# Kernel tuning notes

Hardware: AMD Instinct MI355X
Metric: run time of the kernel (lower is better)

The kernel has to match this reference:

```python
import jax, jax.numpy as jnp
import numpy as np

ALPHA = 5.0
LAMBDA = 1.0


def setup_inputs() -> dict:
    key = jax.random.key(0)
    k1, k2 = jax.random.split(key)
    N, BITS, NCLASS = 2048, 64, 32
    b = jax.random.normal(k1, (N, BITS), dtype=jnp.float32)
    y = jax.random.randint(k2, (N,), 0, NCLASS, dtype=jnp.int32)
    return {"b": b, "y": y}


def reference(b, y):
    # similarity = 0.5 * <b_i, b_j>  -> [N, N]
    sim = 0.5 * (b @ b.T)
    # affinity: same-label pairs (equivalent to onehot(y) @ onehot(y).T > 0)
    aff = y[:, None] == y[None, :]  # [N, N] bool
    N = sim.shape[0]

    def step(carry, i):
        loss_sum, cnt = carry
        pos = aff[i]            # [N] bool, positives for row i
        theta = sim[i]          # [N]
        # triple[p, n] = theta_pos[p] - theta_neg[n] - alpha, clamped
        t = jnp.clip(theta[:, None] - theta[None, :] - ALPHA, -100.0, 50.0)
        # -(t - log(1 + exp(t))) == log1p(exp(t)) - t  (== softplus(-t))
        val = jnp.log1p(jnp.exp(t)) - t
        mask = pos[:, None] & (~pos)[None, :]
        npairs = mask.sum()
        valid = pos.any() & (~pos).any()
        row_loss = jnp.where(
            valid,
            jnp.where(mask, val, 0.0).sum() / jnp.maximum(npairs, 1).astype(val.dtype),
            0.0,
        )
        return (loss_sum + row_loss, cnt + valid.astype(jnp.float32)), None

    init = (jnp.float32(0.0), jnp.float32(0.0))
    (loss_sum, cnt), _ = jax.lax.scan(step, init, jnp.arange(N))
    loss1 = jnp.where(cnt > 0, loss_sum / jnp.maximum(cnt, 1.0), 0.0)
    # quantization loss (sign has zero gradient, same as torch)
    loss2 = jnp.mean((b - jnp.sign(b)) ** 2)
    total = loss1 + LAMBDA * loss2
    return total, loss1, loss2
```

## Files before the change

kernel.cpp:

```cpp
#include <hip/hip_runtime.h>
#include <math.h>

#define NROW 2048
#define BITS 64
#define MB 512
#define RPB 4
#define JQ 4
#define NBLK (NROW / RPB)
#define NWV (MB / 64)
#define MAXPOS 256

#define LN2_F   0.6931471805599453f
#define THSCALE 0.7213475204444817f
#define A_SC    7.213475204444817f

__global__ __launch_bounds__(256) void bt_kernel(const float* __restrict__ b,
                                                 float* __restrict__ bT)
{
    __shared__ float tile[64][65];
    const int t  = threadIdx.x;
    const int j0 = blockIdx.x * 64;
    {
        const int jj = t >> 2, q = t & 3;
        const float4* b4 = reinterpret_cast<const float4*>(b + (size_t)(j0 + jj) * BITS);
#pragma unroll
        for (int m = 0; m < 4; ++m) {
            const float4 v = b4[q * 4 + m];
            const int col = q * 16 + m * 4;
            tile[jj][col + 0] = v.x; tile[jj][col + 1] = v.y;
            tile[jj][col + 2] = v.z; tile[jj][col + 3] = v.w;
        }
    }
    __syncthreads();
    {
        const int k = t >> 2, q = t & 3;
#pragma unroll
        for (int s = 0; s < 4; ++s) {
            float4 v;
            v.x = tile[q * 16 + s * 4 + 0][k];
            v.y = tile[q * 16 + s * 4 + 1][k];
            v.z = tile[q * 16 + s * 4 + 2][k];
            v.w = tile[q * 16 + s * 4 + 3][k];
            *reinterpret_cast<float4*>(&bT[(size_t)k * NROW + j0 + q * 16 + s * 4]) = v;
        }
    }
}

__device__ __forceinline__ float slow4(float e, const float* __restrict__ pp)
{
    float s = 0.f;
#pragma unroll
    for (int k = 0; k < 4; ++k)
        s += __builtin_amdgcn_logf(fmaf(e, pp[k], 1.f));
    return s;
}

template <bool TR>
__global__ __launch_bounds__(MB) void dhn_main(
    const float* __restrict__ b, const float* __restrict__ bT,
    const int* __restrict__ y,
    float* __restrict__ blockLoss, float* __restrict__ blockValid,
    float* __restrict__ blockQ)
{
    const int br  = blockIdx.x;
    const int i0  = br * RPB;
    const int tid = threadIdx.x;
    const int w = tid >> 6, lane = tid & 63;

    __shared__ __align__(16) float  biT[BITS * RPB];
    __shared__ __align__(16) float  posPe[RPB][MAXPOS + 8];
    __shared__ __align__(16) float4 posSG[RPB][MAXPOS / 4 + 2];
    __shared__ int   waveTot[RPB][NWV];
    __shared__ int   waveBase[RPB][NWV];
    __shared__ int   pcnt[RPB];
    __shared__ float wred[NWV], wq[NWV];

    if (tid < BITS * RPB) {
        const int k = tid >> 2, r = tid & 3;
        biT[tid] = b[(size_t)(i0 + r) * BITS + k];
    }
    __syncthreads();

    float th[JQ][RPB] = {};
    if constexpr (TR) {
        const float4* bt4 = reinterpret_cast<const float4*>(bT);
        const float4* bi4 = reinterpret_cast<const float4*>(biT);
#pragma unroll 8
        for (int k = 0; k < BITS; ++k) {
            const float4 bj = bt4[k * (NROW / 4) + tid];
            const float4 bi = bi4[k];
            th[0][0] += bj.x * bi.x; th[0][1] += bj.x * bi.y;
            th[0][2] += bj.x * bi.z; th[0][3] += bj.x * bi.w;
            th[1][0] += bj.y * bi.x; th[1][1] += bj.y * bi.y;
            th[1][2] += bj.y * bi.z; th[1][3] += bj.y * bi.w;
            th[2][0] += bj.z * bi.x; th[2][1] += bj.z * bi.y;
            th[2][2] += bj.z * bi.z; th[2][3] += bj.z * bi.w;
            th[3][0] += bj.w * bi.x; th[3][1] += bj.w * bi.y;
            th[3][2] += bj.w * bi.z; th[3][3] += bj.w * bi.w;
        }
    } else {
        for (int k = 0; k < BITS; ++k) {
#pragma unroll
            for (int q = 0; q < JQ; ++q) {
                const float v = b[(size_t)(4 * tid + q) * BITS + k];
#pragma unroll
                for (int r = 0; r < RPB; ++r) th[q][r] += v * biT[k * 4 + r];
            }
        }
    }

    const int4 y4 = reinterpret_cast<const int4*>(y)[tid];
    const int yj[JQ] = { y4.x, y4.y, y4.z, y4.w };
    int yr[RPB];
#pragma unroll
    for (int r = 0; r < RPB; ++r) yr[r] = y[i0 + r];

    float ev[JQ][RPB];
    int pm[RPB], cnt[RPB];
#pragma unroll
    for (int r = 0; r < RPB; ++r) {
        int m = 0;
#pragma unroll
        for (int q = 0; q < JQ; ++q) {
            const float t2 = th[q][r] * THSCALE;
            const bool f = (yj[q] == yr[r]);
            ev[q][r] = __builtin_amdgcn_exp2f(f ? -t2 : t2 + A_SC);
            if (f) m |= 1 << q;
        }
        pm[r] = m;
        cnt[r] = __popc(m);
    }

    int excl[RPB];
#pragma unroll
    for (int r = 0; r < RPB; ++r) {
        int v = cnt[r];
#pragma unroll
        for (int off = 1; off < 64; off <<= 1) {
            const int t2 = __shfl_up(v, off);
            if (lane >= off) v += t2;
        }
        excl[r] = v - cnt[r];
        if (lane == 63) waveTot[r][w] = v;
    }
    __syncthreads();
    if (tid < RPB) {
        int base = 0;
#pragma unroll
        for (int wv = 0; wv < NWV; ++wv) { waveBase[tid][wv] = base; base += waveTot[tid][wv]; }
        pcnt[tid] = base;
    }
    __syncthreads();

#pragma unroll
    for (int r = 0; r < RPB; ++r) {
        int o = waveBase[r][w] + excl[r];
#pragma unroll
        for (int q = 0; q < JQ; ++q) {
            if ((pm[r] >> q) & 1) {
                if (o < MAXPOS) posPe[r][o] = ev[q][r];
                ++o;
            }
        }
    }
    if (tid < RPB * 8) {
        const int r = tid >> 3, q = tid & 7;
        const int P = pcnt[r] < MAXPOS ? pcnt[r] : MAXPOS;
        const int idx = P + q;
        if (idx < ((P + 7) & ~7)) posPe[r][idx] = 0.f;
    }
    __syncthreads();

    if (tid < RPB * (MAXPOS / 4)) {
        const int r = tid / (MAXPOS / 4);
        const int g = tid % (MAXPOS / 4);
        const int P = pcnt[r] < MAXPOS ? pcnt[r] : MAXPOS;
        const int Ppad = (P + 7) & ~7;
        if (g * 4 < Ppad) {
            float c1 = 0.f, c2 = 0.f, c3 = 0.f, c4 = 0.f;
#pragma unroll
            for (int k = 0; k < 4; ++k) {
                const float p = posPe[r][g * 4 + k];
                c4 = fmaf(p, c3, c4);
                c3 = fmaf(p, c2, c3);
                c2 = fmaf(p, c1, c2);
                c1 += p;
            }
            posSG[r][g] = make_float4(c1, c2, c3, c4);
        }
    }
    __syncthreads();

    float total = 0.f;
#pragma unroll
    for (int r = 0; r < RPB; ++r) {
        const int Pc = pcnt[r];
        const int P  = Pc < MAXPOS ? Pc : MAXPOS;
        const int PG = ((P + 7) & ~7) >> 3;
        float e[JQ];
#pragma unroll
        for (int q = 0; q < JQ; ++q)
            e[q] = ((pm[r] >> q) & 1) ? 0.f : ev[q][r];
        float a[JQ] = {};
        const float4* sg4 = &posSG[r][0];
        const float*  pp  = &posPe[r][0];
        for (int g = 0; g < PG; ++g) {
            const float4 A = sg4[2 * g + 0];
            const float4 B = sg4[2 * g + 1];
#pragma unroll
            for (int q = 0; q < JQ; ++q) {
                const float eq = e[q];
                const float hA = fmaf(fmaf(fmaf(fmaf(A.w, eq, A.z), eq, A.y), eq, A.x), eq, 1.f);
                float lA = __builtin_amdgcn_logf(hA);
                if (__builtin_expect(isinf(hA), 0)) lA = slow4(eq, pp + 8 * g);
                const float hB = fmaf(fmaf(fmaf(fmaf(B.w, eq, B.z), eq, B.y), eq, B.x), eq, 1.f);
                float lB = __builtin_amdgcn_logf(hB);
                if (__builtin_expect(isinf(hB), 0)) lB = slow4(eq, pp + 8 * g + 4);
                a[q] += lA + lB;
            }
        }
        const bool valid = (Pc > 0) && (Pc < NROW);
        const float denom = (float)Pc * (float)(NROW - Pc);
        total += valid ? ((a[0] + a[1]) + (a[2] + a[3])) / denom : 0.f;
    }
    total *= LN2_F;

    float q2 = 0.f;
    if (tid < BITS * RPB) {
        const float x  = biT[tid];
        const float sg = (x > 0.f) ? 1.f : ((x < 0.f) ? -1.f : 0.f);
        const float d  = x - sg;
        q2 = d * d;
    }

#pragma unroll
    for (int off = 32; off > 0; off >>= 1) {
        total += __shfl_xor(total, off);
        q2    += __shfl_xor(q2, off);
    }
    if (lane == 0) { wred[w] = total; wq[w] = q2; }
    __syncthreads();
    if (tid == 0) {
        float tl = 0.f, tq = 0.f;
#pragma unroll
        for (int v = 0; v < NWV; ++v) { tl += wred[v]; tq += wq[v]; }
        blockLoss[br] = tl;
        blockQ[br]    = tq;
        float vc = 0.f;
#pragma unroll
        for (int r = 0; r < RPB; ++r)
            vc += ((pcnt[r] > 0) && (pcnt[r] < NROW)) ? 1.f : 0.f;
        blockValid[br] = vc;
    }
}

__global__ __launch_bounds__(256) void dhn_final_kernel(
    const float* __restrict__ blockLoss, const float* __restrict__ blockValid,
    const float* __restrict__ blockQ, float* __restrict__ out)
{
    const int tid = threadIdx.x;
    const int w = tid >> 6, lane = tid & 63;
    __shared__ float r1[4], r2[4], r3[4];

    float sl = 0.f, sv = 0.f, sq = 0.f;
    for (int i = tid; i < NBLK; i += 256) {
        sl += blockLoss[i]; sv += blockValid[i]; sq += blockQ[i];
    }
#pragma unroll
    for (int off = 32; off > 0; off >>= 1) {
        sl += __shfl_xor(sl, off);
        sv += __shfl_xor(sv, off);
        sq += __shfl_xor(sq, off);
    }
    if (lane == 0) { r1[w] = sl; r2[w] = sv; r3[w] = sq; }
    __syncthreads();
    if (tid == 0) {
        float SL = 0.f, SV = 0.f, SQ = 0.f;
#pragma unroll
        for (int v = 0; v < 4; ++v) { SL += r1[v]; SV += r2[v]; SQ += r3[v]; }
        const float loss1 = (SV > 0.f) ? SL / fmaxf(SV, 1.f) : 0.f;
        const float loss2 = SQ / (float)(NROW * BITS);
        out[0] = loss1 + 1.0f * loss2;
        out[1] = loss1;
        out[2] = loss2;
    }
}

extern "C" void kernel_launch(void* const* d_in, const int* in_sizes, int n_in,
                              void* d_out, int out_size, void* d_ws, size_t ws_size,
                              hipStream_t stream) {
    const float* b = (const float*)d_in[0];
    const int*   y = (const int*)d_in[1];
    float* out = (float*)d_out;

    float* blockLoss  = (float*)d_ws;
    float* blockValid = (float*)((char*)d_ws + 4096);
    float* blockQ     = (float*)((char*)d_ws + 8192);
    float* bT         = (float*)((char*)d_ws + 16384);

    const size_t need = 16384 + (size_t)BITS * NROW * sizeof(float);
    if (ws_size >= need) {
        bt_kernel<<<NROW / 64, 256, 0, stream>>>(b, bT);
        dhn_main<true><<<NBLK, MB, 0, stream>>>(b, bT, y, blockLoss, blockValid, blockQ);
    } else {
        dhn_main<false><<<NBLK, MB, 0, stream>>>(b, nullptr, y, blockLoss, blockValid, blockQ);
    }
    dhn_final_kernel<<<1, 256, 0, stream>>>(blockLoss, blockValid, blockQ, out);
}
```

Before: 42.56 us.

## Batch four log2 evaluations into one via mantissa product and exponent sum

Widens the positive-group size from 8 to 16 and replaces four separate log2 calls per group with one. Each polynomial result is split into an integer exponent and a mantissa in [1,2). The four mantissas are multiplied and a single log2 is taken, while the exponents are summed as integers and corrected at the end. This cuts transcendental instruction count roughly fourfold in the hot loop, at the cost of extra integer/bit operations, more padding work, and a noinline slow fallback covering 16 elements when any value overflows to infinity.

```diff
diff --git a/kernel.cpp b/kernel.cpp
--- a/kernel.cpp
+++ b/kernel.cpp
@@ -46,11 +46,11 @@
     }
 }
 
-__device__ __forceinline__ float slow4(float e, const float* __restrict__ pp)
+__device__ __noinline__ float slow16(float e, const float* __restrict__ pp)
 {
     float s = 0.f;
 #pragma unroll
-    for (int k = 0; k < 4; ++k)
+    for (int k = 0; k < 16; ++k)
         s += __builtin_amdgcn_logf(fmaf(e, pp[k], 1.f));
     return s;
 }
@@ -68,8 +68,8 @@
     const int w = tid >> 6, lane = tid & 63;
 
     __shared__ __align__(16) float  biT[BITS * RPB];
-    __shared__ __align__(16) float  posPe[RPB][MAXPOS + 8];
-    __shared__ __align__(16) float4 posSG[RPB][MAXPOS / 4 + 2];
+    __shared__ __align__(16) float  posPe[RPB][MAXPOS + 16];
+    __shared__ __align__(16) float4 posSG[RPB][MAXPOS / 4 + 4];
     __shared__ int   waveTot[RPB][NWV];
     __shared__ int   waveBase[RPB][NWV];
     __shared__ int   pcnt[RPB];
@@ -163,11 +163,11 @@
             }
         }
     }
-    if (tid < RPB * 8) {
-        const int r = tid >> 3, q = tid & 7;
+    if (tid < RPB * 16) {
+        const int r = tid >> 4, q = tid & 15;
         const int P = pcnt[r] < MAXPOS ? pcnt[r] : MAXPOS;
         const int idx = P + q;
-        if (idx < ((P + 7) & ~7)) posPe[r][idx] = 0.f;
+        if (idx < ((P + 15) & ~15)) posPe[r][idx] = 0.f;
     }
     __syncthreads();
 
@@ -175,7 +175,7 @@
         const int r = tid / (MAXPOS / 4);
         const int g = tid % (MAXPOS / 4);
         const int P = pcnt[r] < MAXPOS ? pcnt[r] : MAXPOS;
-        const int Ppad = (P + 7) & ~7;
+        const int Ppad = (P + 15) & ~15;
         if (g * 4 < Ppad) {
             float c1 = 0.f, c2 = 0.f, c3 = 0.f, c4 = 0.f;
 #pragma unroll
@@ -196,32 +196,52 @@
     for (int r = 0; r < RPB; ++r) {
         const int Pc = pcnt[r];
         const int P  = Pc < MAXPOS ? Pc : MAXPOS;
-        const int PG = ((P + 7) & ~7) >> 3;
+        const int PG = ((P + 15) & ~15) >> 4;
         float e[JQ];
 #pragma unroll
         for (int q = 0; q < JQ; ++q)
             e[q] = ((pm[r] >> q) & 1) ? 0.f : ev[q][r];
         float a[JQ] = {};
+        int   ei[JQ] = {};
         const float4* sg4 = &posSG[r][0];
         const float*  pp  = &posPe[r][0];
         for (int g = 0; g < PG; ++g) {
-            const float4 A = sg4[2 * g + 0];
-            const float4 B = sg4[2 * g + 1];
+            const float4 A = sg4[4 * g + 0];
+            const float4 B = sg4[4 * g + 1];
+            const float4 C = sg4[4 * g + 2];
+            const float4 D = sg4[4 * g + 3];
 #pragma unroll
             for (int q = 0; q < JQ; ++q) {
                 const float eq = e[q];
-                const float hA = fmaf(fmaf(fmaf(fmaf(A.w, eq, A.z), eq, A.y), eq, A.x), eq, 1.f);
-                float lA = __builtin_amdgcn_logf(hA);
-                if (__builtin_expect(isinf(hA), 0)) lA = slow4(eq, pp + 8 * g);
-                const float hB = fmaf(fmaf(fmaf(fmaf(B.w, eq, B.z), eq, B.y), eq, B.x), eq, 1.f);
-                float lB = __builtin_amdgcn_logf(hB);
-                if (__builtin_expect(isinf(hB), 0)) lB = slow4(eq, pp + 8 * g + 4);
-                a[q] += lA + lB;
+                const float h0 = fmaf(fmaf(fmaf(fmaf(A.w, eq, A.z), eq, A.y), eq, A.x), eq, 1.f);
+                const float h1 = fmaf(fmaf(fmaf(fmaf(B.w, eq, B.z), eq, B.y), eq, B.x), eq, 1.f);
+                const float h2 = fmaf(fmaf(fmaf(fmaf(C.w, eq, C.z), eq, C.y), eq, C.x), eq, 1.f);
+                const float h3 = fmaf(fmaf(fmaf(fmaf(D.w, eq, D.z), eq, D.y), eq, D.x), eq, 1.f);
+                const unsigned u0 = __float_as_uint(h0);
+                const unsigned u1 = __float_as_uint(h1);
+                const unsigned u2 = __float_as_uint(h2);
+                const unsigned u3 = __float_as_uint(h3);
+                const float m0 = __uint_as_float((u0 & 0x007FFFFFu) | 0x3F800000u);
+                const float m1 = __uint_as_float((u1 & 0x007FFFFFu) | 0x3F800000u);
+                const float m2 = __uint_as_float((u2 & 0x007FFFFFu) | 0x3F800000u);
+                const float m3 = __uint_as_float((u3 & 0x007FFFFFu) | 0x3F800000u);
+                const unsigned umax = max(max(u0, u1), max(u2, u3));
+                const float mp = (m0 * m1) * (m2 * m3);
+                int ei_iter = (int)((u0 >> 23) + (u1 >> 23)) + (int)((u2 >> 23) + (u3 >> 23));
+                float lg = __builtin_amdgcn_logf(mp);
+                if (__builtin_expect(umax == 0x7F800000u, 0)) {
+                    lg = slow16(eq, pp + 16 * g);
+                    ei_iter = 508;
+                }
+                a[q]  += lg;
+                ei[q] += ei_iter;
             }
         }
         const bool valid = (Pc > 0) && (Pc < NROW);
         const float denom = (float)Pc * (float)(NROW - Pc);
-        total += valid ? ((a[0] + a[1]) + (a[2] + a[3])) / denom : 0.f;
+        const int eisum = ((ei[0] + ei[1]) + (ei[2] + ei[3])) - 2032 * PG;
+        const float rowv = ((a[0] + a[1]) + (a[2] + a[3])) + (float)eisum;
+        total += valid ? rowv / denom : 0.f;
     }
     total *= LN2_F;
 
```

Result: slower. 47.25 us (+11.0%).
